# Kernel tuning notes

Hardware: AMD Instinct MI355X
Metric: run time of the kernel (lower is better)

## Reference

```python
import jax, jax.numpy as jnp
import numpy as np

# Hyperparameters from __init__
TEMPERATURE = 0.07
HARD_POS_W = 1.5
HARD_NEG_W = 2.0
THR_POS = 0.5
THR_NEG = 0.3
NEG_LOSS_W = 0.3

B, D, N_CLASSES = 8192, 256, 1024


def setup_inputs() -> dict:
    key = jax.random.key(0)
    kf, kl = jax.random.split(key)
    features = jax.random.normal(kf, (B, D), dtype=jnp.float32)
    labels = jax.random.randint(kl, (B,), 0, N_CLASSES, dtype=jnp.int32)
    return {"features": features, "labels": labels}


def reference(features, labels):
    b = features.shape[0]
    # L2-normalize features (F.normalize(dim=1))
    anchor = features / jnp.linalg.norm(features, axis=1, keepdims=True)
    sim = anchor @ anchor.T                      # [B, B] cosine similarity
    logits = sim / TEMPERATURE
    logits = logits - jax.lax.stop_gradient(jnp.max(logits, axis=1, keepdims=True))

    mask = (labels[:, None] == labels[None, :]).astype(logits.dtype)   # same-class
    logits_mask = 1.0 - jnp.eye(b, dtype=logits.dtype)                 # exclude self

    # W2ML weights: computed from detached similarities (torch used .item())
    sim_d = jax.lax.stop_gradient(sim)
    offdiag = logits_mask > 0
    is_pos = mask > 0
    hard_pos = is_pos & (sim_d < THR_POS) & offdiag
    pos_weights = jnp.where(
        hard_pos, 1.0 + (THR_POS - sim_d) / THR_POS * (HARD_POS_W - 1.0), 1.0)
    hard_neg = (~is_pos) & (sim_d > THR_NEG) & offdiag
    neg_weights = jnp.where(
        hard_neg, 1.0 + (sim_d - THR_NEG) / (1.0 - THR_NEG) * (HARD_NEG_W - 1.0), 1.0)

    # SupCon log-prob with self excluded from the denominator
    exp_logits = jnp.exp(logits) * logits_mask
    denom = jnp.sum(exp_logits, axis=1, keepdims=True)
    log_prob = logits - jnp.log(denom)

    pos_mask = mask * logits_mask
    pos_cnt = jnp.clip(jnp.sum(pos_mask, axis=1), 1.0, None)
    positive_loss = -jnp.mean(
        jnp.sum(pos_mask * pos_weights * log_prob, axis=1) / pos_cnt)

    # Negative term: weighted mean probability mass assigned to negatives
    neg_mask = (1.0 - mask) * logits_mask
    neg_cnt = jnp.clip(jnp.sum(neg_mask, axis=1), 1.0, None)
    prob = exp_logits / denom
    negative_loss = jnp.mean(
        jnp.sum(neg_mask * neg_weights * prob, axis=1) / neg_cnt)

    return positive_loss + NEG_LOSS_W * negative_loss
```

## Files before the change

kernel.cpp:

```cpp
#include <hip/hip_runtime.h>

#define BSZ  8192
#define DDIM 256
#define BM 128
#define BN 128
#define NT   64
#define NTRI (NT * (NT + 1) / 2)

typedef float f32x4 __attribute__((ext_vector_type(4)));
typedef short bf16x8 __attribute__((ext_vector_type(8)));

__device__ __forceinline__ unsigned short f32_to_bf16(float f) {
    unsigned int u = __float_as_uint(f);
    u += 0x7fffu + ((u >> 16) & 1u);
    return (unsigned short)(u >> 16);
}

#if __has_builtin(__builtin_amdgcn_exp2f)
__device__ __forceinline__ float fast_exp2(float x) { return __builtin_amdgcn_exp2f(x); }
#else
__device__ __forceinline__ float fast_exp2(float x) {
    float r;
    asm("v_exp_f32 %0, %1" : "=v"(r) : "v"(x));
    return r;
}
#endif

#define K_E1   20.60992915555662f
#define K_E2  -20.60992915555662f
#define K_INVT 14.285714285714286f
#define K_N1   1.4285714285714286f
#define K_N2   0.5714285714285714f

template<int CTRL>
__device__ __forceinline__ float dpp_add(float v) {
    int t = __builtin_amdgcn_update_dpp(0, __float_as_int(v), CTRL, 0xF, 0xF, true);
    return v + __int_as_float(t);
}
__device__ __forceinline__ float red16(float v) {
    v = dpp_add<0xB1>(v);
    v = dpp_add<0x4E>(v);
    v = dpp_add<0x141>(v);
    v = dpp_add<0x140>(v);
    return v;
}

__device__ __forceinline__ int swz(int b) {
    return b ^ ((((b >> 7) ^ (b >> 10)) & 7) << 4);
}

__device__ __forceinline__ void decode_tile(int t, int& It, int& Jt) {
    const int off1 = 136, off2 = 392, off3 = 648, off4 = 904, off5 = 1040,
              off6 = 1296, off7 = 1552, off8 = 1688, off9 = 1944;
    int b = (t >= off1) + (t >= off2) + (t >= off3) + (t >= off4) + (t >= off5)
          + (t >= off6) + (t >= off7) + (t >= off8) + (t >= off9);
    int si, sj, r0;
    switch (b) {
        case 0: si = 0; sj = 0; r0 = 0;    break;
        case 1: si = 0; sj = 1; r0 = off1; break;
        case 2: si = 0; sj = 2; r0 = off2; break;
        case 3: si = 0; sj = 3; r0 = off3; break;
        case 4: si = 1; sj = 1; r0 = off4; break;
        case 5: si = 1; sj = 2; r0 = off5; break;
        case 6: si = 1; sj = 3; r0 = off6; break;
        case 7: si = 2; sj = 2; r0 = off7; break;
        case 8: si = 2; sj = 3; r0 = off8; break;
        default: si = 3; sj = 3; r0 = off9; break;
    }
    const int rr = t - r0;
    int il, jl;
    if (si == sj) {
        il = 0;
        #pragma unroll
        for (int q = 1; q < 16; q++) if (rr >= (16 * q - (q * (q - 1)) / 2)) il = q;
        jl = il + (rr - (16 * il - (il * (il - 1)) / 2));
    } else {
        il = rr >> 4;
        jl = rr & 15;
    }
    It = si * 16 + il;
    Jt = sj * 16 + jl;
}

__global__ __launch_bounds__(256) void norm_kernel(const float* __restrict__ feat,
                                                   unsigned short* __restrict__ anchorT,
                                                   float* __restrict__ posAcc,
                                                   unsigned int* __restrict__ counter) {
    __shared__ __align__(16) unsigned short img[8 * 512];
    char* const imgb = (char*)img;
    const int tid  = threadIdx.x;
    const int wid  = tid >> 6;
    const int lane = tid & 63;
    const int R    = blockIdx.x;
    const int R0   = R * 16;

    if (tid < 64) posAcc[blockIdx.x * 64 + tid] = 0.0f;
    if (blockIdx.x == 0 && tid == 0) *counter = 0u;

    #pragma unroll
    for (int it = 0; it < 4; it++) {
        const int row = R0 + it * 4 + wid;
        const float4 v = ((const float4*)(feat + (size_t)row * DDIM))[lane];
        float ss = v.x * v.x + v.y * v.y + v.z * v.z + v.w * v.w;
        #pragma unroll
        for (int off = 32; off > 0; off >>= 1) ss += __shfl_xor(ss, off, 64);
        const float inv = rsqrtf(ss);
        ushort4 o;
        o.x = f32_to_bf16(v.x * inv);
        o.y = f32_to_bf16(v.y * inv);
        o.z = f32_to_bf16(v.z * inv);
        o.w = f32_to_bf16(v.w * inv);
        const int C    = lane >> 3;
        const int l16  = (row & 15) + (((lane >> 1) & 3) << 4);
        const int wb   = (C << 10) + (l16 << 4) + ((lane & 1) << 3);
        *(ushort4*)(imgb + swz(wb)) = o;
    }
    __syncthreads();
    #pragma unroll
    for (int p = 0; p < 2; p++) {
        const int c = p * 4 + wid;
        *(bf16x8*)(anchorT + ((size_t)(c * 512 + R)) * 512 + lane * 8) =
            *(const bf16x8*)(imgb + swz((c << 10) + (lane << 4)));
    }
}

__device__ __forceinline__ void gload_lds16(const unsigned short* g, unsigned short* l) {
    __builtin_amdgcn_global_load_lds(
        (const __attribute__((address_space(1))) void*)g,
        (__attribute__((address_space(3))) void*)l, 16, 0, 0);
}

__global__ __launch_bounds__(512, 4) void simloss_kernel(
    const unsigned short* __restrict__ anchorT,
    const int* __restrict__ labels,
    float* __restrict__ part,
    float* __restrict__ posAcc)
{
    __shared__ __align__(16) unsigned short As[8 * 512];
    __shared__ __align__(16) unsigned short As2[8 * 512];
    __shared__ __align__(16) unsigned short Bs[8 * 512];
    __shared__ __align__(16) unsigned short Bs2[8 * 512];
    float* const rowDT = (float*)As;
    float* const colDT = (float*)Bs;

    int It, Jt;
    decode_tile(blockIdx.x, It, Jt);
    const bool diag = (It == Jt);
    const int I0 = It * BM, J0 = Jt * BN;

    const int tid  = threadIdx.x;
    const int lane = tid & 63;
    const int w    = tid >> 6;
    const int rw   = w >> 1;
    const int cw   = w & 1;
    const int cl   = lane & 15;
    const int rg   = lane >> 4;
    const int laneOff = lane * 8;

    f32x4 acc[2][4];
    #pragma unroll
    for (int f = 0; f < 2; f++)
        #pragma unroll
        for (int g = 0; g < 4; g++)
            acc[f][g] = (f32x4){0.f, 0.f, 0.f, 0.f};

    const unsigned short* aSrc = anchorT + (size_t)It * 4096 + tid * 8;
    const unsigned short* bSrc = anchorT + (size_t)Jt * 4096 + tid * 8;
    unsigned short* const aD0 = &As[w * 512];
    unsigned short* const aD1 = &As2[w * 512];
    unsigned short* const bD0 = &Bs[w * 512];
    unsigned short* const bD1 = &Bs2[w * 512];

    gload_lds16(aSrc, aD0);
    gload_lds16(bSrc, bD0);

    #pragma unroll
    for (int c = 0; c < 8; c++) {
        if (c < 7) {
            const size_t off = (size_t)(c + 1) * 262144;
            gload_lds16(aSrc + off, ((c + 1) & 1) ? aD1 : aD0);
            gload_lds16(bSrc + off, ((c + 1) & 1) ? bD1 : bD0);
            asm volatile("s_waitcnt vmcnt(2)" ::: "memory");
        } else {
            asm volatile("s_waitcnt vmcnt(0)" ::: "memory");
        }
        __builtin_amdgcn_s_barrier();
        __builtin_amdgcn_sched_barrier(0);

        const unsigned short* aB = ((c & 1) ? As2 : As) + (rw * 2) * 512 + laneOff;
        const unsigned short* bB = ((c & 1) ? Bs2 : Bs) + (cw * 4) * 512 + laneOff;
        const bf16x8 a0 = *(const bf16x8*)(aB);
        const bf16x8 a1 = *(const bf16x8*)(aB + 512);
        const bf16x8 b0 = *(const bf16x8*)(bB);
        const bf16x8 b1 = *(const bf16x8*)(bB + 512);
        const bf16x8 b2 = *(const bf16x8*)(bB + 1024);
        const bf16x8 b3 = *(const bf16x8*)(bB + 1536);
        acc[0][0] = __builtin_amdgcn_mfma_f32_16x16x32_bf16(a0, b0, acc[0][0], 0, 0, 0);
        acc[0][1] = __builtin_amdgcn_mfma_f32_16x16x32_bf16(a0, b1, acc[0][1], 0, 0, 0);
        acc[0][2] = __builtin_amdgcn_mfma_f32_16x16x32_bf16(a0, b2, acc[0][2], 0, 0, 0);
        acc[0][3] = __builtin_amdgcn_mfma_f32_16x16x32_bf16(a0, b3, acc[0][3], 0, 0, 0);
        acc[1][0] = __builtin_amdgcn_mfma_f32_16x16x32_bf16(a1, b0, acc[1][0], 0, 0, 0);
        acc[1][1] = __builtin_amdgcn_mfma_f32_16x16x32_bf16(a1, b1, acc[1][1], 0, 0, 0);
        acc[1][2] = __builtin_amdgcn_mfma_f32_16x16x32_bf16(a1, b2, acc[1][2], 0, 0, 0);
        acc[1][3] = __builtin_amdgcn_mfma_f32_16x16x32_bf16(a1, b3, acc[1][3], 0, 0, 0);

        if (c < 7) {
            asm volatile("s_waitcnt lgkmcnt(0)" ::: "memory");
            __builtin_amdgcn_s_barrier();
        }
    }

    int lj[4];
    #pragma unroll
    for (int g = 0; g < 4; g++) lj[g] = labels[J0 + cw * 64 + g * 16 + cl];

    float m8[8];
    #pragma unroll
    for (int f = 0; f < 2; f++)
        #pragma unroll
        for (int g = 0; g < 4; g++) {
            const f32x4 c = acc[f][g];
            m8[f * 4 + g] = fmaxf(fmaxf(c[0], c[1]), fmaxf(c[2], c[3]));
        }
    const float mx = fmaxf(fmaxf(fmaxf(m8[0], m8[1]), fmaxf(m8[2], m8[3])),
                           fmaxf(fmaxf(m8[4], m8[5]), fmaxf(m8[6], m8[7])));
    const bool needW = __any(fmaf(mx, K_N1, K_N2) > 1.0f) != 0;

    float cd[4] = {0.f, 0.f, 0.f, 0.f};

    #pragma unroll
    for (int f = 0; f < 2; f++) {
        float rd[4] = {0.f, 0.f, 0.f, 0.f};
        const int rbase = I0 + rw * 32 + f * 16 + rg * 4;
        const int4 lv = *(const int4*)(labels + rbase);
        const int li[4] = {lv.x, lv.y, lv.z, lv.w};
        #pragma unroll
        for (int g = 0; g < 4; g++) {
            const int lj_ = lj[g];
            const bool granule = (rw * 2 + f) == (cw * 4 + g);
            const f32x4 c = acc[f][g];
            #pragma unroll
            for (int r = 0; r < 4; r++) {
                const float s = c[r];
                const bool self = diag && granule && ((rg * 4 + r) == cl);
                const float e  = self ? 0.f : fast_exp2(fmaf(s, K_E1, K_E2));
                rd[r] += e;
                if (!diag) cd[g] += e;
                if (li[r] == lj_ && !self) {
                    const float wn = fmaxf(fmaf(s, K_N1, K_N2), 1.0f);
                    const float we = wn * e;
                    const float wp = fmaxf(1.5f - s, 1.0f);
                    const float slp = fmaf(s, K_INVT, -K_INVT) * wp;
                    float* pi = posAcc + (size_t)(rbase + r) * 4;
                    atomicAdd(pi + 0, slp);
                    atomicAdd(pi + 1, wp);
                    atomicAdd(pi + 2, we);
                    atomicAdd(pi + 3, 1.0f);
                    if (!diag) {
                        float* pj = posAcc + (size_t)(J0 + cw * 64 + g * 16 + cl) * 4;
                        atomicAdd(pj + 0, slp);
                        atomicAdd(pj + 1, wp);
                        atomicAdd(pj + 2, we);
                        atomicAdd(pj + 3, 1.0f);
                    }
                }
            }
        }
        float rt[4];
        if (!needW) {
            #pragma unroll
            for (int r = 0; r < 4; r++) rt[r] = rd[r];
        } else {
            #pragma unroll
            for (int r = 0; r < 4; r++) rt[r] = 0.f;
            #pragma unroll
            for (int g = 0; g < 4; g++) {
                const bool granule = (rw * 2 + f) == (cw * 4 + g);
                const f32x4 c = acc[f][g];
                #pragma unroll
                for (int r = 0; r < 4; r++) {
                    const float s = c[r];
                    const bool self = diag && granule && ((rg * 4 + r) == cl);
                    const float e  = self ? 0.f : fast_exp2(fmaf(s, K_E1, K_E2));
                    const float wn = fmaxf(fmaf(s, K_N1, K_N2), 1.0f);
                    rt[r] += wn * e;
                }
            }
        }
        #pragma unroll
        for (int r = 0; r < 4; r++) {
            rd[r] = red16(rd[r]);
            rt[r] = red16(rt[r]);
        }
        if (cl == 0) {
            #pragma unroll
            for (int r = 0; r < 4; r++) {
                const int row = rw * 32 + f * 16 + rg * 4 + r;
                rowDT[(cw * BM + row) * 2 + 0] = rd[r];
                rowDT[(cw * BM + row) * 2 + 1] = rt[r];
            }
        }
    }

    if (!diag) {
        float ct[4];
        if (!needW) {
            #pragma unroll
            for (int g = 0; g < 4; g++) ct[g] = cd[g];
        } else {
            #pragma unroll
            for (int g = 0; g < 4; g++) ct[g] = 0.f;
            #pragma unroll
            for (int f = 0; f < 2; f++)
                #pragma unroll
                for (int g = 0; g < 4; g++) {
                    const f32x4 c = acc[f][g];
                    #pragma unroll
                    for (int r = 0; r < 4; r++) {
                        const float s = c[r];
                        const float e  = fast_exp2(fmaf(s, K_E1, K_E2));
                        const float wn = fmaxf(fmaf(s, K_N1, K_N2), 1.0f);
                        ct[g] += wn * e;
                    }
                }
        }
        #pragma unroll
        for (int g = 0; g < 4; g++) {
            cd[g] += __shfl_xor(cd[g], 16, 64);
            cd[g] += __shfl_xor(cd[g], 32, 64);
            ct[g] += __shfl_xor(ct[g], 16, 64);
            ct[g] += __shfl_xor(ct[g], 32, 64);
        }
        if (rg == 0) {
            #pragma unroll
            for (int g = 0; g < 4; g++) {
                const int col = cw * 64 + g * 16 + cl;
                colDT[(rw * BN + col) * 2 + 0] = cd[g];
                colDT[(rw * BN + col) * 2 + 1] = ct[g];
            }
        }
    }

    __syncthreads();
    if (tid < BM) {
        float2 v;
        v.x = rowDT[(0 * BM + tid) * 2 + 0] + rowDT[(1 * BM + tid) * 2 + 0];
        v.y = rowDT[(0 * BM + tid) * 2 + 1] + rowDT[(1 * BM + tid) * 2 + 1];
        ((float2*)part)[(size_t)Jt * BSZ + I0 + tid] = v;
    } else if (tid < 2 * BM && !diag) {
        const int c = tid - BM;
        float2 v;
        v.x = colDT[(0 * BN + c) * 2 + 0] + colDT[(1 * BN + c) * 2 + 0]
            + colDT[(2 * BN + c) * 2 + 0] + colDT[(3 * BN + c) * 2 + 0];
        v.y = colDT[(0 * BN + c) * 2 + 1] + colDT[(1 * BN + c) * 2 + 1]
            + colDT[(2 * BN + c) * 2 + 1] + colDT[(3 * BN + c) * 2 + 1];
        ((float2*)part)[(size_t)It * BSZ + J0 + c] = v;
    }
}

__global__ __launch_bounds__(256) void reduce_final_kernel(
    const float* __restrict__ part, const float* __restrict__ posAcc,
    double* __restrict__ partial, unsigned int* __restrict__ counter,
    float* __restrict__ out)
{
    const int t   = threadIdx.x;
    const int row = blockIdx.x * 32 + (t >> 3);
    const int sg  = t & 7;
    float dsum = 0.f, T2 = 0.f;
    const float2* p2 = (const float2*)part;
    #pragma unroll
    for (int j = 0; j < 8; j++) {
        const float2 v = p2[(size_t)(sg * 8 + j) * BSZ + row];
        dsum += v.x; T2 += v.y;
    }
    #pragma unroll
    for (int off = 1; off < 8; off <<= 1) {
        dsum += __shfl_xor(dsum, off, 64);
        T2   += __shfl_xor(T2,   off, 64);
    }
    __shared__ double sp[32], sn[32];
    if (sg == 0) {
        const float4 pa = ((const float4*)posAcc)[row];
        const float s1 = pa.x, w1 = pa.y, s2 = T2 - pa.z, cnt = pa.w;
        const float pc = fmaxf(cnt, 1.0f);
        const float nc = fmaxf(8191.0f - cnt, 1.0f);
        const float ld = logf(dsum);
        sp[t >> 3] = (double)((s1 - ld * w1) / pc);
        sn[t >> 3] = (double)((s2 / dsum) / nc);
    }
    __syncthreads();
    __shared__ bool amLast;
    if (t < 32) {
        double p = sp[t], n = sn[t];
        #pragma unroll
        for (int off = 1; off < 32; off <<= 1) {
            p += __shfl_xor(p, off, 64);
            n += __shfl_xor(n, off, 64);
        }
        if (t == 0) {
            partial[blockIdx.x * 2 + 0] = p;
            partial[blockIdx.x * 2 + 1] = n;
            __threadfence();
            amLast = (atomicAdd(counter, 1u) == 255u);
        }
    }
    __syncthreads();
    if (amLast) {
        __threadfence();
        __shared__ double fp[256], fn[256];
        volatile double* vp = (volatile double*)partial;
        fp[t] = vp[t * 2 + 0];
        fn[t] = vp[t * 2 + 1];
        __syncthreads();
        for (int s = 128; s > 0; s >>= 1) {
            if (t < s) { fp[t] += fp[t + s]; fn[t] += fn[t + s]; }
            __syncthreads();
        }
        if (t == 0) out[0] = (float)(-fp[0] / (double)BSZ + 0.3 * (fn[0] / (double)BSZ));
    }
}

extern "C" void kernel_launch(void* const* d_in, const int* in_sizes, int n_in,
                              void* d_out, int out_size, void* d_ws, size_t ws_size,
                              hipStream_t stream) {
    const float* feat = (const float*)d_in[0];
    const int* labels = (const int*)d_in[1];
    float* out = (float*)d_out;

    char* ws = (char*)d_ws;
    unsigned short* anchorT = (unsigned short*)ws;
    const size_t anchorBytes = (size_t)BSZ * DDIM * sizeof(unsigned short);
    float* part = (float*)(ws + anchorBytes);
    const size_t partBytes = (size_t)NT * BSZ * 2 * sizeof(float);
    float* posAcc = (float*)(ws + anchorBytes + partBytes);
    const size_t posBytes = (size_t)BSZ * 4 * sizeof(float);
    double* partial = (double*)(ws + anchorBytes + partBytes + posBytes);
    unsigned int* counter = (unsigned int*)(ws + anchorBytes + partBytes + posBytes + 4096);

    norm_kernel<<<BSZ / 16, 256, 0, stream>>>(feat, anchorT, posAcc, counter);
    simloss_kernel<<<NTRI, 512, 0, stream>>>(anchorT, labels, part, posAcc);
    reduce_final_kernel<<<BSZ / 32, 256, 0, stream>>>(part, posAcc, partial, counter, out);
}
```

Measured before the change: 113.6 us.

## Enlarge similarity tiles to 256x256 with triple-buffered LDS staging

Doubles the block tile to 256x256, so each warp computes a 128x64 sub-tile with 32 MFMA accumulators. The change cuts the number of triangle tiles, redundant operand loads and partial-sum writes, and halves the partial rows the final reduction reads. The LDS pipeline becomes triple-buffered, which lets the per-chunk second barrier go. In exchange register pressure rises and occupancy drops to 2 blocks per CU. With 528 tiles against roughly 512 resident slots, a small second wave of blocks may form a tail.

```diff
diff --git a/kernel.cpp b/kernel.cpp
--- a/kernel.cpp
+++ b/kernel.cpp
@@ -2,9 +2,9 @@
 
 #define BSZ  8192
 #define DDIM 256
-#define BM 128
-#define BN 128
-#define NT   64
+#define BM 256
+#define BN 256
+#define NT   32
 #define NTRI (NT * (NT + 1) / 2)
 
 typedef float f32x4 __attribute__((ext_vector_type(4)));
@@ -50,23 +50,12 @@
 }
 
 __device__ __forceinline__ void decode_tile(int t, int& It, int& Jt) {
-    const int off1 = 136, off2 = 392, off3 = 648, off4 = 904, off5 = 1040,
-              off6 = 1296, off7 = 1552, off8 = 1688, off9 = 1944;
-    int b = (t >= off1) + (t >= off2) + (t >= off3) + (t >= off4) + (t >= off5)
-          + (t >= off6) + (t >= off7) + (t >= off8) + (t >= off9);
+    const int off1 = 136, off2 = 392;
+    const int b = (t >= off1) + (t >= off2);
     int si, sj, r0;
-    switch (b) {
-        case 0: si = 0; sj = 0; r0 = 0;    break;
-        case 1: si = 0; sj = 1; r0 = off1; break;
-        case 2: si = 0; sj = 2; r0 = off2; break;
-        case 3: si = 0; sj = 3; r0 = off3; break;
-        case 4: si = 1; sj = 1; r0 = off4; break;
-        case 5: si = 1; sj = 2; r0 = off5; break;
-        case 6: si = 1; sj = 3; r0 = off6; break;
-        case 7: si = 2; sj = 2; r0 = off7; break;
-        case 8: si = 2; sj = 3; r0 = off8; break;
-        default: si = 3; sj = 3; r0 = off9; break;
-    }
+    if (b == 0)      { si = 0; sj = 0; r0 = 0;    }
+    else if (b == 1) { si = 0; sj = 1; r0 = off1; }
+    else             { si = 1; sj = 1; r0 = off2; }
     const int rr = t - r0;
     int il, jl;
     if (si == sj) {
@@ -130,18 +119,16 @@
         (__attribute__((address_space(3))) void*)l, 16, 0, 0);
 }
 
-__global__ __launch_bounds__(512, 4) void simloss_kernel(
+__global__ __launch_bounds__(512, 2) void simloss_kernel(
     const unsigned short* __restrict__ anchorT,
     const int* __restrict__ labels,
     float* __restrict__ part,
     float* __restrict__ posAcc)
 {
-    __shared__ __align__(16) unsigned short As[8 * 512];
-    __shared__ __align__(16) unsigned short As2[8 * 512];
-    __shared__ __align__(16) unsigned short Bs[8 * 512];
-    __shared__ __align__(16) unsigned short Bs2[8 * 512];
-    float* const rowDT = (float*)As;
-    float* const colDT = (float*)Bs;
+    __shared__ __align__(16) unsigned short Abuf[3][8192];
+    __shared__ __align__(16) unsigned short Bbuf[3][8192];
+    float* const rowDT = (float*)Abuf;
+    float* const colDT = (float*)Bbuf;
 
     int It, Jt;
     decode_tile(blockIdx.x, It, Jt);
@@ -151,97 +138,88 @@
     const int tid  = threadIdx.x;
     const int lane = tid & 63;
     const int w    = tid >> 6;
-    const int rw   = w >> 1;
-    const int cw   = w & 1;
+    const int rw   = w >> 2;
+    const int cw   = w & 3;
     const int cl   = lane & 15;
     const int rg   = lane >> 4;
     const int laneOff = lane * 8;
 
-    f32x4 acc[2][4];
-    #pragma unroll
-    for (int f = 0; f < 2; f++)
+    f32x4 acc[8][4];
+    #pragma unroll
+    for (int t = 0; t < 8; t++)
         #pragma unroll
         for (int g = 0; g < 4; g++)
-            acc[f][g] = (f32x4){0.f, 0.f, 0.f, 0.f};
-
-    const unsigned short* aSrc = anchorT + (size_t)It * 4096 + tid * 8;
-    const unsigned short* bSrc = anchorT + (size_t)Jt * 4096 + tid * 8;
-    unsigned short* const aD0 = &As[w * 512];
-    unsigned short* const aD1 = &As2[w * 512];
-    unsigned short* const bD0 = &Bs[w * 512];
-    unsigned short* const bD1 = &Bs2[w * 512];
-
-    gload_lds16(aSrc, aD0);
-    gload_lds16(bSrc, bD0);
+            acc[t][g] = (f32x4){0.f, 0.f, 0.f, 0.f};
+
+    #define STAGE(c, b)                                                              \
+        do {                                                                         \
+            const size_t ga = ((size_t)(c) * 512 + It * 16) * 512;                   \
+            const size_t gb = ((size_t)(c) * 512 + Jt * 16) * 512;                   \
+            gload_lds16(anchorT + ga + tid * 8,        &Abuf[b][w * 512]);           \
+            gload_lds16(anchorT + ga + 4096 + tid * 8, &Abuf[b][4096 + w * 512]);    \
+            gload_lds16(anchorT + gb + tid * 8,        &Bbuf[b][w * 512]);           \
+            gload_lds16(anchorT + gb + 4096 + tid * 8, &Bbuf[b][4096 + w * 512]);    \
+        } while (0)
+
+    STAGE(0, 0);
 
     #pragma unroll
     for (int c = 0; c < 8; c++) {
         if (c < 7) {
-            const size_t off = (size_t)(c + 1) * 262144;
-            gload_lds16(aSrc + off, ((c + 1) & 1) ? aD1 : aD0);
-            gload_lds16(bSrc + off, ((c + 1) & 1) ? bD1 : bD0);
-            asm volatile("s_waitcnt vmcnt(2)" ::: "memory");
+            STAGE(c + 1, (c + 1) % 3);
+            asm volatile("s_waitcnt vmcnt(4)" ::: "memory");
         } else {
             asm volatile("s_waitcnt vmcnt(0)" ::: "memory");
         }
         __builtin_amdgcn_s_barrier();
         __builtin_amdgcn_sched_barrier(0);
 
-        const unsigned short* aB = ((c & 1) ? As2 : As) + (rw * 2) * 512 + laneOff;
-        const unsigned short* bB = ((c & 1) ? Bs2 : Bs) + (cw * 4) * 512 + laneOff;
-        const bf16x8 a0 = *(const bf16x8*)(aB);
-        const bf16x8 a1 = *(const bf16x8*)(aB + 512);
-        const bf16x8 b0 = *(const bf16x8*)(bB);
-        const bf16x8 b1 = *(const bf16x8*)(bB + 512);
-        const bf16x8 b2 = *(const bf16x8*)(bB + 1024);
-        const bf16x8 b3 = *(const bf16x8*)(bB + 1536);
-        acc[0][0] = __builtin_amdgcn_mfma_f32_16x16x32_bf16(a0, b0, acc[0][0], 0, 0, 0);
-        acc[0][1] = __builtin_amdgcn_mfma_f32_16x16x32_bf16(a0, b1, acc[0][1], 0, 0, 0);
-        acc[0][2] = __builtin_amdgcn_mfma_f32_16x16x32_bf16(a0, b2, acc[0][2], 0, 0, 0);
-        acc[0][3] = __builtin_amdgcn_mfma_f32_16x16x32_bf16(a0, b3, acc[0][3], 0, 0, 0);
-        acc[1][0] = __builtin_amdgcn_mfma_f32_16x16x32_bf16(a1, b0, acc[1][0], 0, 0, 0);
-        acc[1][1] = __builtin_amdgcn_mfma_f32_16x16x32_bf16(a1, b1, acc[1][1], 0, 0, 0);
-        acc[1][2] = __builtin_amdgcn_mfma_f32_16x16x32_bf16(a1, b2, acc[1][2], 0, 0, 0);
-        acc[1][3] = __builtin_amdgcn_mfma_f32_16x16x32_bf16(a1, b3, acc[1][3], 0, 0, 0);
-
-        if (c < 7) {
-            asm volatile("s_waitcnt lgkmcnt(0)" ::: "memory");
-            __builtin_amdgcn_s_barrier();
-        }
-    }
+        const int bc = c % 3;
+        const unsigned short* aB = &Abuf[bc][(rw * 8) * 512 + laneOff];
+        const unsigned short* bB = &Bbuf[bc][(cw * 4) * 512 + laneOff];
+        bf16x8 a[8], bb[4];
+        #pragma unroll
+        for (int t = 0; t < 8; t++) a[t] = *(const bf16x8*)(aB + t * 512);
+        #pragma unroll
+        for (int g = 0; g < 4; g++) bb[g] = *(const bf16x8*)(bB + g * 512);
+        #pragma unroll
+        for (int t = 0; t < 8; t++)
+            #pragma unroll
+            for (int g = 0; g < 4; g++)
+                acc[t][g] = __builtin_amdgcn_mfma_f32_16x16x32_bf16(a[t], bb[g], acc[t][g], 0, 0, 0);
+    }
+    #undef STAGE
 
     int lj[4];
     #pragma unroll
     for (int g = 0; g < 4; g++) lj[g] = labels[J0 + cw * 64 + g * 16 + cl];
 
-    float m8[8];
-    #pragma unroll
-    for (int f = 0; f < 2; f++)
+    float mx = -1e30f;
+    #pragma unroll
+    for (int t = 0; t < 8; t++)
         #pragma unroll
         for (int g = 0; g < 4; g++) {
-            const f32x4 c = acc[f][g];
-            m8[f * 4 + g] = fmaxf(fmaxf(c[0], c[1]), fmaxf(c[2], c[3]));
-        }
-    const float mx = fmaxf(fmaxf(fmaxf(m8[0], m8[1]), fmaxf(m8[2], m8[3])),
-                           fmaxf(fmaxf(m8[4], m8[5]), fmaxf(m8[6], m8[7])));
+            const f32x4 c4 = acc[t][g];
+            mx = fmaxf(mx, fmaxf(fmaxf(c4[0], c4[1]), fmaxf(c4[2], c4[3])));
+        }
     const bool needW = __any(fmaf(mx, K_N1, K_N2) > 1.0f) != 0;
 
     float cd[4] = {0.f, 0.f, 0.f, 0.f};
 
     #pragma unroll
-    for (int f = 0; f < 2; f++) {
+    for (int t = 0; t < 8; t++) {
         float rd[4] = {0.f, 0.f, 0.f, 0.f};
-        const int rbase = I0 + rw * 32 + f * 16 + rg * 4;
+        const int rbase = I0 + rw * 128 + t * 16 + rg * 4;
         const int4 lv = *(const int4*)(labels + rbase);
         const int li[4] = {lv.x, lv.y, lv.z, lv.w};
         #pragma unroll
         for (int g = 0; g < 4; g++) {
             const int lj_ = lj[g];
-            const bool granule = (rw * 2 + f) == (cw * 4 + g);
-            const f32x4 c = acc[f][g];
+            const bool granule = (rw * 8 + t) == (cw * 4 + g);
+            const f32x4 c4 = acc[t][g];
             #pragma unroll
             for (int r = 0; r < 4; r++) {
-                const float s = c[r];
+                const float s = c4[r];
                 const bool self = diag && granule && ((rg * 4 + r) == cl);
                 const float e  = self ? 0.f : fast_exp2(fmaf(s, K_E1, K_E2));
                 rd[r] += e;
@@ -275,11 +253,11 @@
             for (int r = 0; r < 4; r++) rt[r] = 0.f;
             #pragma unroll
             for (int g = 0; g < 4; g++) {
-                const bool granule = (rw * 2 + f) == (cw * 4 + g);
-                const f32x4 c = acc[f][g];
+                const bool granule = (rw * 8 + t) == (cw * 4 + g);
+                const f32x4 c4 = acc[t][g];
                 #pragma unroll
                 for (int r = 0; r < 4; r++) {
-                    const float s = c[r];
+                    const float s = c4[r];
                     const bool self = diag && granule && ((rg * 4 + r) == cl);
                     const float e  = self ? 0.f : fast_exp2(fmaf(s, K_E1, K_E2));
                     const float wn = fmaxf(fmaf(s, K_N1, K_N2), 1.0f);
@@ -295,7 +273,7 @@
         if (cl == 0) {
             #pragma unroll
             for (int r = 0; r < 4; r++) {
-                const int row = rw * 32 + f * 16 + rg * 4 + r;
+                const int row = rw * 128 + t * 16 + rg * 4 + r;
                 rowDT[(cw * BM + row) * 2 + 0] = rd[r];
                 rowDT[(cw * BM + row) * 2 + 1] = rt[r];
             }
@@ -311,13 +289,13 @@
             #pragma unroll
             for (int g = 0; g < 4; g++) ct[g] = 0.f;
             #pragma unroll
-            for (int f = 0; f < 2; f++)
+            for (int t = 0; t < 8; t++)
                 #pragma unroll
                 for (int g = 0; g < 4; g++) {
-                    const f32x4 c = acc[f][g];
+                    const f32x4 c4 = acc[t][g];
                     #pragma unroll
                     for (int r = 0; r < 4; r++) {
-                        const float s = c[r];
+                        const float s = c4[r];
                         const float e  = fast_exp2(fmaf(s, K_E1, K_E2));
                         const float wn = fmaxf(fmaf(s, K_N1, K_N2), 1.0f);
                         ct[g] += wn * e;
@@ -344,16 +322,16 @@
     __syncthreads();
     if (tid < BM) {
         float2 v;
-        v.x = rowDT[(0 * BM + tid) * 2 + 0] + rowDT[(1 * BM + tid) * 2 + 0];
-        v.y = rowDT[(0 * BM + tid) * 2 + 1] + rowDT[(1 * BM + tid) * 2 + 1];
+        v.x = rowDT[(0 * BM + tid) * 2 + 0] + rowDT[(1 * BM + tid) * 2 + 0]
+            + rowDT[(2 * BM + tid) * 2 + 0] + rowDT[(3 * BM + tid) * 2 + 0];
+        v.y = rowDT[(0 * BM + tid) * 2 + 1] + rowDT[(1 * BM + tid) * 2 + 1]
+            + rowDT[(2 * BM + tid) * 2 + 1] + rowDT[(3 * BM + tid) * 2 + 1];
         ((float2*)part)[(size_t)Jt * BSZ + I0 + tid] = v;
-    } else if (tid < 2 * BM && !diag) {
+    } else if (!diag) {
         const int c = tid - BM;
         float2 v;
-        v.x = colDT[(0 * BN + c) * 2 + 0] + colDT[(1 * BN + c) * 2 + 0]
-            + colDT[(2 * BN + c) * 2 + 0] + colDT[(3 * BN + c) * 2 + 0];
-        v.y = colDT[(0 * BN + c) * 2 + 1] + colDT[(1 * BN + c) * 2 + 1]
-            + colDT[(2 * BN + c) * 2 + 1] + colDT[(3 * BN + c) * 2 + 1];
+        v.x = colDT[(0 * BN + c) * 2 + 0] + colDT[(1 * BN + c) * 2 + 0];
+        v.y = colDT[(0 * BN + c) * 2 + 1] + colDT[(1 * BN + c) * 2 + 1];
         ((float2*)part)[(size_t)It * BSZ + J0 + c] = v;
     }
 }
@@ -369,8 +347,8 @@
     float dsum = 0.f, T2 = 0.f;
     const float2* p2 = (const float2*)part;
     #pragma unroll
-    for (int j = 0; j < 8; j++) {
-        const float2 v = p2[(size_t)(sg * 8 + j) * BSZ + row];
+    for (int j = 0; j < 4; j++) {
+        const float2 v = p2[(size_t)(sg * 4 + j) * BSZ + row];
         dsum += v.x; T2 += v.y;
     }
     #pragma unroll
```

Result: slower. 139.8 us (+23.1%).
